# Kernel tuning notes

Measured on AMD Instinct MI355X. Metric: run time of the kernel, lower is better.

The kernel has to match this reference:

```python
import jax, jax.numpy as jnp
import numpy as np

D_MODEL = 1024
NUM_HEADS = 16
HEAD_DIM = D_MODEL // NUM_HEADS


def setup_inputs() -> dict:
    key = jax.random.key(0)
    ks = jax.random.split(key, 5)
    B, S, D_IN = 2, 2048, 1024
    x = jax.random.normal(ks[0], (B, S, D_IN), dtype=jnp.float32)
    std = 0.02
    wq = jax.random.normal(ks[1], (D_MODEL, D_IN), dtype=jnp.float32) * std
    wk = jax.random.normal(ks[2], (D_MODEL, D_IN), dtype=jnp.float32) * std
    wv = jax.random.normal(ks[3], (D_MODEL, D_IN), dtype=jnp.float32) * std
    wo = jax.random.normal(ks[4], (D_IN, D_MODEL), dtype=jnp.float32) * std
    return {"x": x, "wq": wq, "wk": wk, "wv": wv, "wo": wo}


def _mha(x, wq, wk, wv, wo):
    B, S, _ = x.shape
    H, Dh = NUM_HEADS, HEAD_DIM
    # projections: Linear applies x @ W.T with W of shape [out, in]
    q = (x @ wq.T).reshape(B, S, H, Dh).transpose(0, 2, 1, 3)  # [B,H,S,Dh]
    k = (x @ wk.T).reshape(B, S, H, Dh).transpose(0, 2, 1, 3)
    v = (x @ wv.T).reshape(B, S, H, Dh).transpose(0, 2, 1, 3)
    scores = jnp.einsum('bhqd,bhkd->bhqk', q, k) / jnp.sqrt(jnp.float32(Dh))
    causal = jnp.tril(jnp.ones((S, S), dtype=bool))  # True where attended
    scores = jnp.where(causal, scores, -jnp.inf)
    attn = jax.nn.softmax(scores, axis=-1)
    out = jnp.einsum('bhqk,bhkd->bhqd', attn, v)  # [B,H,S,Dh]
    out = out.transpose(0, 2, 1, 3).reshape(B, S, H * Dh)
    return out @ wo.T


def reference(x, wq, wk, wv, wo):
    return _mha(x, wq, wk, wv, wo)
```

## Files before the change

### kernel.cpp

```cpp
#include <hip/hip_runtime.h>
#include <hip/hip_bf16.h>
#include <stdint.h>

using bf16 = __hip_bfloat16;
typedef __attribute__((ext_vector_type(4))) short shorts4;
typedef __attribute__((ext_vector_type(8))) short short8;
typedef __attribute__((ext_vector_type(4))) float floatx4;
typedef __attribute__((ext_vector_type(4))) unsigned int uintx4;

constexpr int BATCH = 2;
constexpr int SEQ   = 2048;
constexpr int NH    = 16;
constexpr int DH    = 64;
constexpr int DM    = 1024;
constexpr int MROWS = BATCH * SEQ;
constexpr int OUTN  = MROWS * DM;
constexpr int WN    = DM * DM;

__device__ inline short bfbits(float x) {
    bf16 h = __float2bfloat16(x);
    return __builtin_bit_cast(short, h);
}

__device__ inline void async16(bf16* lds, const bf16* g) {
    __builtin_amdgcn_global_load_lds(
        (const __attribute__((address_space(1))) unsigned int*)g,
        (__attribute__((address_space(3))) unsigned int*)lds, 16, 0, 0);
}

__device__ inline void cvt8(const float* src, bf16* dst) {
    float4 f0 = *(const float4*)(src);
    float4 f1 = *(const float4*)(src + 4);
    short8 o;
    o[0] = bfbits(f0.x); o[1] = bfbits(f0.y); o[2] = bfbits(f0.z); o[3] = bfbits(f0.w);
    o[4] = bfbits(f1.x); o[5] = bfbits(f1.y); o[6] = bfbits(f1.z); o[7] = bfbits(f1.w);
    *(short8*)(dst) = o;
}

__global__ __launch_bounds__(256)
void cvt_all(const float* __restrict__ x,  const float* __restrict__ wq,
             const float* __restrict__ wk, const float* __restrict__ wv,
             const float* __restrict__ wo, bf16* __restrict__ dst,
             bf16* __restrict__ wob)
{
    const size_t i = ((size_t)blockIdx.x * 256 + threadIdx.x) * 8;
    if (i < (size_t)OUTN + 3 * WN) {
        const float* src; size_t off;
        if (i < (size_t)OUTN)               { src = x;  off = i; }
        else if (i < (size_t)OUTN + WN)     { src = wq; off = i - OUTN; }
        else if (i < (size_t)OUTN + 2 * WN) { src = wk; off = i - OUTN - WN; }
        else                                { src = wv; off = i - OUTN - 2 * (size_t)WN; }
        cvt8(src + off, dst + i);
    } else {
        const size_t off = i - OUTN - 3 * (size_t)WN;
        cvt8(wo + off, wob + off);
    }
}

__global__ __launch_bounds__(256)
void cvt_inputs(const float* __restrict__ x,  const float* __restrict__ wq,
                const float* __restrict__ wk, const float* __restrict__ wv,
                bf16* __restrict__ dst)
{
    const size_t i = ((size_t)blockIdx.x * 256 + threadIdx.x) * 8;
    const float* src; size_t off;
    if (i < (size_t)OUTN)               { src = x;  off = i; }
    else if (i < (size_t)OUTN + WN)     { src = wq; off = i - OUTN; }
    else if (i < (size_t)OUTN + 2 * WN) { src = wk; off = i - OUTN - WN; }
    else                                { src = wv; off = i - OUTN - 2 * (size_t)WN; }
    cvt8(src + off, dst + i);
}

__global__ __launch_bounds__(256)
void cvt_wo(const float* __restrict__ wo, bf16* __restrict__ dst)
{
    const size_t i = ((size_t)blockIdx.x * 256 + threadIdx.x) * 8;
    cvt8(wo + i, dst + i);
}

template<int MODE, int NT>
__global__ __launch_bounds__(256)
void gemm_mfma(const bf16* __restrict__ A,
               const bf16* __restrict__ W0, const bf16* __restrict__ W1,
               const bf16* __restrict__ W2,
               bf16* __restrict__ C0, bf16* __restrict__ C1, bf16* __restrict__ C2,
               float* __restrict__ F)
{
    constexpr int NJ = NT / 32;
    __shared__ __align__(16) bf16 As[128 * 32];
    __shared__ __align__(16) bf16 Ws[NT * 32];

    const int t    = threadIdx.x;
    const int wave = t >> 6;
    const int lane = t & 63;
    const int quad = lane >> 4;
    const int l16  = lane & 15;
    const int m0 = blockIdx.y * 128;
    const int n0 = blockIdx.x * NT;
    const int wr = (wave >> 1) * 64;
    const int wc = (wave & 1) * (NT / 2);

    const int z = (MODE == 0) ? blockIdx.z : 0;
    const bf16* W = (z == 0) ? W0 : ((z == 1) ? W1 : W2);

    const int c    = t;
    bf16* lA0 = As + c * 8;          bf16* lA1 = As + c * 8 + 2048;
    bf16* lW0 = Ws + c * 8;          bf16* lW1 = Ws + c * 8 + 2048;
    const int ar0 = m0 + (c >> 2),  ar1 = m0 + 64 + (c >> 2);
    const int nr0 = n0 + (c >> 2),  nr1 = n0 + 64 + (c >> 2);
    const int kc  = (c & 3) * 8;

    floatx4 acc[4][NJ] = {};

    for (int k0 = 0; k0 < DM; k0 += 32) {
        const bf16* gA0 = A + (size_t)ar0 * DM + k0 + kc;
        const bf16* gA1 = A + (size_t)ar1 * DM + k0 + kc;
        const bf16* gW0 = W + (size_t)nr0 * DM + k0 + kc;
        const bf16* gW1 = W + (size_t)nr1 * DM + k0 + kc;

        __syncthreads();
        async16(lA0, gA0);
        async16(lA1, gA1);
        async16(lW0, gW0);
        if (NT == 128) async16(lW1, gW1);
        __syncthreads();

        short8 af[4], wf[NJ];
        #pragma unroll
        for (int i = 0; i < 4; i++)
            af[i] = *(const short8*)(As + (wr + i * 16 + l16) * 32 + quad * 8);
        #pragma unroll
        for (int j = 0; j < NJ; j++)
            wf[j] = *(const short8*)(Ws + (wc + j * 16 + l16) * 32 + quad * 8);
        #pragma unroll
        for (int i = 0; i < 4; i++)
            #pragma unroll
            for (int j = 0; j < NJ; j++)
                acc[i][j] = __builtin_amdgcn_mfma_f32_16x16x32_bf16(af[i], wf[j], acc[i][j], 0, 0, 0);
    }

    #pragma unroll
    for (int i = 0; i < 4; i++) {
        #pragma unroll
        for (int j = 0; j < NJ; j++) {
            if (MODE == 0 && z == 2) {
                const int s0 = m0 + wr + i * 16 + quad * 4;
                const int gn = n0 + wc + j * 16 + l16;
                const int b = s0 >> 11, sr = s0 & (SEQ - 1);
                const int h = gn >> 6,  d = gn & (DH - 1);
                shorts4 pv;
                #pragma unroll
                for (int r = 0; r < 4; r++) pv[r] = bfbits(acc[i][j][r]);
                *(shorts4*)(C2 + (((size_t)(b * NH + h)) * DH + d) * SEQ + sr) = pv;
            } else {
                #pragma unroll
                for (int r = 0; r < 4; r++) {
                    const int gm = m0 + wr + i * 16 + quad * 4 + r;
                    const int gn = n0 + wc + j * 16 + l16;
                    if (MODE == 1) {
                        F[(size_t)gm * DM + gn] = acc[i][j][r];
                    } else {
                        float av = acc[i][j][r];
                        if (z == 0) av *= 0.18033688f;
                        bf16* dst = (z == 0) ? C0 : C1;
                        dst[(size_t)gm * DM + gn] = __float2bfloat16(av);
                    }
                }
            }
        }
    }
}

__global__ __launch_bounds__(256)
void attn_flash(bf16* __restrict__ Q, const bf16* __restrict__ K,
                const bf16* __restrict__ Vt)
{
    __shared__ __align__(16) bf16 Ks[128 * 64];
    __shared__ __align__(16) bf16 Vs[64 * 128];

    const int t    = threadIdx.x;
    const int wave = t >> 6;
    const int lane = t & 63;
    const int quad = lane >> 4;
    const int l16  = lane & 15;

    const int h  = blockIdx.y;
    const int b  = blockIdx.z;
    const int qt = (blockIdx.x + 5 * h + 16 * b) & 31;
    const int q0 = qt * 64;
    const int hc = h * DH;
    const size_t rowb = (size_t)b * SEQ;
    const size_t bhv  = ((size_t)(b * NH + h)) * SEQ * DH;

    const int qrow = q0 + wave * 16;
    const int qg   = qrow + l16;

    short8 qf0 = *(const short8*)(Q + (rowb + qrow + l16) * DM + hc + quad * 8);
    short8 qf1 = *(const short8*)(Q + (rowb + qrow + l16) * DM + hc + quad * 8 + 32);

    floatx4 oacc[4] = {};
    float lsum = 0.f;

    const int kx   = l16 & 7;
    const int koff0 = (quad ^ kx) * 8;
    const int koff1 = ((quad ^ 4) ^ kx) * 8;

    const int sA = (2 * (quad & 1)) * 16 + l16;
    const int sB = sA + 16;
    const bool hiTile = (quad >= 2);

    for (int k0 = 0; k0 < q0 + 64; k0 += 128) {
        __syncthreads();
        #pragma unroll
        for (int p = 0; p < 4; p++) {
            const int ck = p * 256 + t;
            const int kr = ck >> 3;
            const int kg = (ck & 7) ^ (kr & 7);
            async16(Ks + ck * 8, K + (rowb + k0 + kr) * DM + hc + kg * 8);
            const int cv = p * 256 + t;
            const int vr = cv >> 4;
            const int vg = (cv & 15) ^ (vr & 15);
            async16(Vs + cv * 8, Vt + bhv + (size_t)vr * SEQ + k0 + vg * 8);
        }
        __syncthreads();

        #pragma unroll
        for (int c64 = 0; c64 < 128; c64 += 64) {
            const int kb0 = k0 + c64;
            if (kb0 > qrow + 15) continue;

            floatx4 sc[4];
            #pragma unroll
            for (int jj = 0; jj < 4; jj++) {
                const int rowk = c64 + jj * 16 + l16;
                short8 kf0 = *(const short8*)(Ks + rowk * 64 + koff0);
                short8 kf1 = *(const short8*)(Ks + rowk * 64 + koff1);
                floatx4 cc = {};
                cc = __builtin_amdgcn_mfma_f32_16x16x32_bf16(kf0, qf0, cc, 0, 0, 0);
                cc = __builtin_amdgcn_mfma_f32_16x16x32_bf16(kf1, qf1, cc, 0, 0, 0);
                sc[jj] = cc;
            }
            if (kb0 + 63 > qrow) {
                #pragma unroll
                for (int jj = 0; jj < 4; jj++) {
                    const int kgb = kb0 + jj * 16 + quad * 4;
                    #pragma unroll
                    for (int r = 0; r < 4; r++)
                        sc[jj][r] = (kgb + r <= qg) ? sc[jj][r] : -1e30f;
                }
            }
            #pragma unroll
            for (int jj = 0; jj < 4; jj++)
                #pragma unroll
                for (int r = 0; r < 4; r++) {
                    const float p = __builtin_amdgcn_exp2f(sc[jj][r]);
                    sc[jj][r] = p;
                    lsum += p;
                }

            unsigned lo[4], hi[4];
            #pragma unroll
            for (int jj = 0; jj < 4; jj++) {
                lo[jj] = (unsigned)(unsigned short)bfbits(sc[jj][0]) |
                         ((unsigned)(unsigned short)bfbits(sc[jj][1]) << 16);
                hi[jj] = (unsigned)(unsigned short)bfbits(sc[jj][2]) |
                         ((unsigned)(unsigned short)bfbits(sc[jj][3]) << 16);
            }
            #pragma unroll
            for (int ks = 0; ks < 2; ks++) {
                unsigned d0a = __shfl((int)lo[2 * ks],     sA, 64);
                unsigned d0b = __shfl((int)lo[2 * ks + 1], sA, 64);
                unsigned d1a = __shfl((int)hi[2 * ks],     sA, 64);
                unsigned d1b = __shfl((int)hi[2 * ks + 1], sA, 64);
                unsigned d2a = __shfl((int)lo[2 * ks],     sB, 64);
                unsigned d2b = __shfl((int)lo[2 * ks + 1], sB, 64);
                unsigned d3a = __shfl((int)hi[2 * ks],     sB, 64);
                unsigned d3b = __shfl((int)hi[2 * ks + 1], sB, 64);
                uintx4 pw;
                pw[0] = hiTile ? d0b : d0a;
                pw[1] = hiTile ? d1b : d1a;
                pw[2] = hiTile ? d2b : d2a;
                pw[3] = hiTile ? d3b : d3a;
                short8 pb = __builtin_bit_cast(short8, pw);
                #pragma unroll
                for (int td = 0; td < 4; td++) {
                    const int vrow = td * 16 + l16;
                    const int vg   = ((c64 >> 3) + ks * 4 + quad) ^ l16;
                    short8 vf = *(const short8*)(Vs + vrow * 128 + vg * 8);
                    oacc[td] = __builtin_amdgcn_mfma_f32_16x16x32_bf16(vf, pb, oacc[td], 0, 0, 0);
                }
            }
        }
    }

    lsum += __shfl_xor(lsum, 16, 64);
    lsum += __shfl_xor(lsum, 32, 64);

    __syncthreads();
    bf16* T = Vs + wave * 16 * 72;
    const float invl = 1.0f / lsum;
    #pragma unroll
    for (int td = 0; td < 4; td++)
        #pragma unroll
        for (int r = 0; r < 4; r++)
            T[l16 * 72 + td * 16 + quad * 4 + r] = __float2bfloat16(oacc[td][r] * invl);
    #pragma unroll
    for (int pass = 0; pass < 2; pass++) {
        const int rq = (lane >> 3) + pass * 8;
        const int dd = (lane & 7) * 8;
        short8 v8 = *(const short8*)(T + rq * 72 + dd);
        *(short8*)(Q + (rowb + qrow + rq) * DM + hc + dd) = v8;
    }
}

extern "C" void kernel_launch(void* const* d_in, const int* in_sizes, int n_in,
                              void* d_out, int out_size, void* d_ws, size_t ws_size,
                              hipStream_t stream)
{
    const float* x  = (const float*)d_in[0];
    const float* wq = (const float*)d_in[1];
    const float* wk = (const float*)d_in[2];
    const float* wv = (const float*)d_in[3];
    const float* wo = (const float*)d_in[4];
    float* out = (float*)d_out;

    bf16* qb = (bf16*)d_ws;
    bf16* kb = qb + (size_t)OUTN;
    bf16* vb = kb + (size_t)OUTN;

    bf16* xb  = (bf16*)d_out;
    bf16* wqb = xb + (size_t)OUTN;
    bf16* wkb = wqb + WN;
    bf16* wvb = wkb + WN;

    const bool wsBig = ws_size >= (size_t)(3 * (size_t)OUTN + WN) * sizeof(bf16);

    if (wsBig) {
        bf16* wob = vb + (size_t)OUTN;
        cvt_all<<<(OUTN + 4 * WN) / (8 * 256), 256, 0, stream>>>(
            x, wq, wk, wv, wo, xb, wob);
        gemm_mfma<0, 128><<<dim3(DM / 128, MROWS / 128, 3), dim3(256), 0, stream>>>(
            xb, wqb, wkb, wvb, qb, kb, vb, nullptr);
        attn_flash<<<dim3(SEQ / 64, NH, BATCH), dim3(256), 0, stream>>>(qb, kb, vb);
        gemm_mfma<1, 64><<<dim3(DM / 64, MROWS / 128, 1), dim3(256), 0, stream>>>(
            qb, wob, nullptr, nullptr, nullptr, nullptr, nullptr, out);
    } else {
        cvt_inputs<<<(OUTN + 3 * WN) / (8 * 256), 256, 0, stream>>>(x, wq, wk, wv, xb);
        gemm_mfma<0, 128><<<dim3(DM / 128, MROWS / 128, 3), dim3(256), 0, stream>>>(
            xb, wqb, wkb, wvb, qb, kb, vb, nullptr);
        attn_flash<<<dim3(SEQ / 64, NH, BATCH), dim3(256), 0, stream>>>(qb, kb, vb);
        bf16* wob = kb;
        cvt_wo<<<WN / (8 * 256), 256, 0, stream>>>(wo, wob);
        gemm_mfma<1, 64><<<dim3(DM / 64, MROWS / 128, 1), dim3(256), 0, stream>>>(
            qb, wob, nullptr, nullptr, nullptr, nullptr, nullptr, out);
    }
}
```

Measured before the change: 185.6 us.

## Switch attention to 32x32x16 MFMA with 128-row query tiles per block

The attention kernel moves from 16x16x32 to 32x32x16 bf16 MFMA tiles. Each wave now handles 32 query rows, so a block covers 128 queries, which halves the grid and doubles K/V tile reuse per LDS load. The P-matrix relayout becomes a single xor-32 lane swap instead of eight indexed shuffles. The trade-offs are coarser causal skipping, fewer blocks (512) for occupancy and load balance, and higher accumulator register use.

```diff
diff --git a/kernel.cpp b/kernel.cpp
--- a/kernel.cpp
+++ b/kernel.cpp
@@ -6,6 +6,7 @@
 typedef __attribute__((ext_vector_type(4))) short shorts4;
 typedef __attribute__((ext_vector_type(8))) short short8;
 typedef __attribute__((ext_vector_type(4))) float floatx4;
+typedef __attribute__((ext_vector_type(16))) float floatx16;
 typedef __attribute__((ext_vector_type(4))) unsigned int uintx4;
 
 constexpr int BATCH = 2;
@@ -20,6 +21,11 @@
 __device__ inline short bfbits(float x) {
     bf16 h = __float2bfloat16(x);
     return __builtin_bit_cast(short, h);
+}
+
+__device__ inline unsigned pack2(float a, float b) {
+    return (unsigned)(unsigned short)bfbits(a) |
+           ((unsigned)(unsigned short)bfbits(b) << 16);
 }
 
 __device__ inline void async16(bf16* lds, const bf16* g) {
@@ -175,41 +181,36 @@
 void attn_flash(bf16* __restrict__ Q, const bf16* __restrict__ K,
                 const bf16* __restrict__ Vt)
 {
-    __shared__ __align__(16) bf16 Ks[128 * 64];
-    __shared__ __align__(16) bf16 Vs[64 * 128];
+    __shared__ __align__(16) bf16 smem[16384];
+    bf16* Ks = smem;
+    bf16* Vs = smem + 8192;
 
     const int t    = threadIdx.x;
     const int wave = t >> 6;
     const int lane = t & 63;
-    const int quad = lane >> 4;
-    const int l16  = lane & 15;
+    const int hi   = lane >> 5;
+    const int l32  = lane & 31;
 
     const int h  = blockIdx.y;
     const int b  = blockIdx.z;
-    const int qt = (blockIdx.x + 5 * h + 16 * b) & 31;
-    const int q0 = qt * 64;
+    const int qt = (blockIdx.x + 5 * h + 8 * b) & 15;
+    const int q0 = qt * 128;
     const int hc = h * DH;
     const size_t rowb = (size_t)b * SEQ;
     const size_t bhv  = ((size_t)(b * NH + h)) * SEQ * DH;
 
-    const int qrow = q0 + wave * 16;
-    const int qg   = qrow + l16;
-
-    short8 qf0 = *(const short8*)(Q + (rowb + qrow + l16) * DM + hc + quad * 8);
-    short8 qf1 = *(const short8*)(Q + (rowb + qrow + l16) * DM + hc + quad * 8 + 32);
-
-    floatx4 oacc[4] = {};
+    const int qrow = q0 + wave * 32;
+    const int qg   = qrow + l32;
+
+    short8 qf[4];
+    #pragma unroll
+    for (int s = 0; s < 4; s++)
+        qf[s] = *(const short8*)(Q + (rowb + qg) * DM + hc + s * 16 + hi * 8);
+
+    floatx16 oacc[2] = {};
     float lsum = 0.f;
 
-    const int kx   = l16 & 7;
-    const int koff0 = (quad ^ kx) * 8;
-    const int koff1 = ((quad ^ 4) ^ kx) * 8;
-
-    const int sA = (2 * (quad & 1)) * 16 + l16;
-    const int sB = sA + 16;
-    const bool hiTile = (quad >= 2);
-
-    for (int k0 = 0; k0 < q0 + 64; k0 += 128) {
+    for (int k0 = 0; k0 < q0 + 128; k0 += 128) {
         __syncthreads();
         #pragma unroll
         for (int p = 0; p < 4; p++) {
@@ -217,96 +218,99 @@
             const int kr = ck >> 3;
             const int kg = (ck & 7) ^ (kr & 7);
             async16(Ks + ck * 8, K + (rowb + k0 + kr) * DM + hc + kg * 8);
-            const int cv = p * 256 + t;
-            const int vr = cv >> 4;
-            const int vg = (cv & 15) ^ (vr & 15);
-            async16(Vs + cv * 8, Vt + bhv + (size_t)vr * SEQ + k0 + vg * 8);
+            const int vr = ck >> 4;
+            const int vg = (ck & 15) ^ (vr & 15);
+            async16(Vs + ck * 8, Vt + bhv + (size_t)vr * SEQ + k0 + vg * 8);
         }
         __syncthreads();
 
         #pragma unroll
         for (int c64 = 0; c64 < 128; c64 += 64) {
             const int kb0 = k0 + c64;
-            if (kb0 > qrow + 15) continue;
-
-            floatx4 sc[4];
+            if (kb0 > qrow + 31) continue;
+
             #pragma unroll
-            for (int jj = 0; jj < 4; jj++) {
-                const int rowk = c64 + jj * 16 + l16;
-                short8 kf0 = *(const short8*)(Ks + rowk * 64 + koff0);
-                short8 kf1 = *(const short8*)(Ks + rowk * 64 + koff1);
-                floatx4 cc = {};
-                cc = __builtin_amdgcn_mfma_f32_16x16x32_bf16(kf0, qf0, cc, 0, 0, 0);
-                cc = __builtin_amdgcn_mfma_f32_16x16x32_bf16(kf1, qf1, cc, 0, 0, 0);
-                sc[jj] = cc;
-            }
-            if (kb0 + 63 > qrow) {
-                #pragma unroll
-                for (int jj = 0; jj < 4; jj++) {
-                    const int kgb = kb0 + jj * 16 + quad * 4;
+            for (int kt = 0; kt < 2; kt++) {
+                const int kb = kb0 + kt * 32;
+                if (kb > qrow + 31) continue;
+
+                const int krow = c64 + kt * 32 + l32;
+                floatx16 sc = {};
+                #pragma unroll
+                for (int s = 0; s < 4; s++) {
+                    const int g = (s * 2 + hi) ^ (krow & 7);
+                    short8 kf = *(const short8*)(Ks + krow * 64 + g * 8);
+                    sc = __builtin_amdgcn_mfma_f32_32x32x16_bf16(kf, qf[s], sc, 0, 0, 0);
+                }
+
+                if (kb + 31 > qrow) {
                     #pragma unroll
-                    for (int r = 0; r < 4; r++)
-                        sc[jj][r] = (kgb + r <= qg) ? sc[jj][r] : -1e30f;
-                }
-            }
-            #pragma unroll
-            for (int jj = 0; jj < 4; jj++)
-                #pragma unroll
-                for (int r = 0; r < 4; r++) {
-                    const float p = __builtin_amdgcn_exp2f(sc[jj][r]);
-                    sc[jj][r] = p;
+                    for (int r = 0; r < 16; r++) {
+                        const int key = kb + (r & 3) + 8 * (r >> 2) + 4 * hi;
+                        sc[r] = (key <= qg) ? sc[r] : -1e30f;
+                    }
+                }
+
+                #pragma unroll
+                for (int r = 0; r < 16; r++) {
+                    const float p = __builtin_amdgcn_exp2f(sc[r]);
+                    sc[r] = p;
                     lsum += p;
                 }
 
-            unsigned lo[4], hi[4];
-            #pragma unroll
-            for (int jj = 0; jj < 4; jj++) {
-                lo[jj] = (unsigned)(unsigned short)bfbits(sc[jj][0]) |
-                         ((unsigned)(unsigned short)bfbits(sc[jj][1]) << 16);
-                hi[jj] = (unsigned)(unsigned short)bfbits(sc[jj][2]) |
-                         ((unsigned)(unsigned short)bfbits(sc[jj][3]) << 16);
-            }
-            #pragma unroll
-            for (int ks = 0; ks < 2; ks++) {
-                unsigned d0a = __shfl((int)lo[2 * ks],     sA, 64);
-                unsigned d0b = __shfl((int)lo[2 * ks + 1], sA, 64);
-                unsigned d1a = __shfl((int)hi[2 * ks],     sA, 64);
-                unsigned d1b = __shfl((int)hi[2 * ks + 1], sA, 64);
-                unsigned d2a = __shfl((int)lo[2 * ks],     sB, 64);
-                unsigned d2b = __shfl((int)lo[2 * ks + 1], sB, 64);
-                unsigned d3a = __shfl((int)hi[2 * ks],     sB, 64);
-                unsigned d3b = __shfl((int)hi[2 * ks + 1], sB, 64);
-                uintx4 pw;
-                pw[0] = hiTile ? d0b : d0a;
-                pw[1] = hiTile ? d1b : d1a;
-                pw[2] = hiTile ? d2b : d2a;
-                pw[3] = hiTile ? d3b : d3a;
-                short8 pb = __builtin_bit_cast(short8, pw);
-                #pragma unroll
-                for (int td = 0; td < 4; td++) {
-                    const int vrow = td * 16 + l16;
-                    const int vg   = ((c64 >> 3) + ks * 4 + quad) ^ l16;
-                    short8 vf = *(const short8*)(Vs + vrow * 128 + vg * 8);
-                    oacc[td] = __builtin_amdgcn_mfma_f32_16x16x32_bf16(vf, pb, oacc[td], 0, 0, 0);
+                unsigned d[4][2];
+                #pragma unroll
+                for (int g = 0; g < 4; g++) {
+                    d[g][0] = pack2(sc[4 * g + 0], sc[4 * g + 1]);
+                    d[g][1] = pack2(sc[4 * g + 2], sc[4 * g + 3]);
+                }
+
+                #pragma unroll
+                for (int h16 = 0; h16 < 2; h16++) {
+                    const unsigned a0 = d[h16 * 2][0],     a1 = d[h16 * 2][1];
+                    const unsigned b0 = d[h16 * 2 + 1][0], b1 = d[h16 * 2 + 1][1];
+                    const unsigned mine0 = hi ? b0 : a0, mine1 = hi ? b1 : a1;
+                    const unsigned give0 = hi ? a0 : b0, give1 = hi ? a1 : b1;
+                    const unsigned r0 = (unsigned)__shfl_xor((int)give0, 32, 64);
+                    const unsigned r1 = (unsigned)__shfl_xor((int)give1, 32, 64);
+                    uintx4 pw;
+                    pw[0] = hi ? r0 : mine0;
+                    pw[1] = hi ? r1 : mine1;
+                    pw[2] = hi ? mine0 : r0;
+                    pw[3] = hi ? mine1 : r1;
+                    short8 pb = __builtin_bit_cast(short8, pw);
+
+                    const int Gbase = (c64 >> 3) + kt * 4 + h16 * 2 + hi;
+                    #pragma unroll
+                    for (int tile = 0; tile < 2; tile++) {
+                        const int vrow = tile * 32 + l32;
+                        const int vg = Gbase ^ (vrow & 15);
+                        short8 vf = *(const short8*)(Vs + vrow * 128 + vg * 8);
+                        oacc[tile] = __builtin_amdgcn_mfma_f32_32x32x16_bf16(vf, pb, oacc[tile], 0, 0, 0);
+                    }
                 }
             }
         }
     }
 
-    lsum += __shfl_xor(lsum, 16, 64);
     lsum += __shfl_xor(lsum, 32, 64);
+    const float invl = 1.0f / lsum;
 
     __syncthreads();
-    bf16* T = Vs + wave * 16 * 72;
-    const float invl = 1.0f / lsum;
+    bf16* T = smem + wave * (32 * 72);
     #pragma unroll
-    for (int td = 0; td < 4; td++)
-        #pragma unroll
-        for (int r = 0; r < 4; r++)
-            T[l16 * 72 + td * 16 + quad * 4 + r] = __float2bfloat16(oacc[td][r] * invl);
+    for (int tile = 0; tile < 2; tile++)
+        #pragma unroll
+        for (int rq = 0; rq < 4; rq++) {
+            shorts4 v4;
+            #pragma unroll
+            for (int s = 0; s < 4; s++) v4[s] = bfbits(oacc[tile][rq * 4 + s] * invl);
+            *(shorts4*)(T + l32 * 72 + tile * 32 + rq * 8 + hi * 4) = v4;
+        }
+    asm volatile("s_waitcnt lgkmcnt(0)" ::: "memory");
     #pragma unroll
-    for (int pass = 0; pass < 2; pass++) {
-        const int rq = (lane >> 3) + pass * 8;
+    for (int p = 0; p < 4; p++) {
+        const int rq = (lane >> 3) + p * 8;
         const int dd = (lane & 7) * 8;
         short8 v8 = *(const short8*)(T + rq * 72 + dd);
         *(short8*)(Q + (rowb + qrow + rq) * DM + hc + dd) = v8;
@@ -341,14 +345,14 @@
             x, wq, wk, wv, wo, xb, wob);
         gemm_mfma<0, 128><<<dim3(DM / 128, MROWS / 128, 3), dim3(256), 0, stream>>>(
             xb, wqb, wkb, wvb, qb, kb, vb, nullptr);
-        attn_flash<<<dim3(SEQ / 64, NH, BATCH), dim3(256), 0, stream>>>(qb, kb, vb);
+        attn_flash<<<dim3(SEQ / 128, NH, BATCH), dim3(256), 0, stream>>>(qb, kb, vb);
         gemm_mfma<1, 64><<<dim3(DM / 64, MROWS / 128, 1), dim3(256), 0, stream>>>(
             qb, wob, nullptr, nullptr, nullptr, nullptr, nullptr, out);
     } else {
         cvt_inputs<<<(OUTN + 3 * WN) / (8 * 256), 256, 0, stream>>>(x, wq, wk, wv, xb);
         gemm_mfma<0, 128><<<dim3(DM / 128, MROWS / 128, 3), dim3(256), 0, stream>>>(
             xb, wqb, wkb, wvb, qb, kb, vb, nullptr);
-        attn_flash<<<dim3(SEQ / 64, NH, BATCH), dim3(256), 0, stream>>>(qb, kb, vb);
+        attn_flash<<<dim3(SEQ / 128, NH, BATCH), dim3(256), 0, stream>>>(qb, kb, vb);
         bf16* wob = kb;
         cvt_wo<<<WN / (8 * 256), 256, 0, stream>>>(wo, wob);
         gemm_mfma<1, 64><<<dim3(DM / 64, MROWS / 128, 1), dim3(256), 0, stream>>>(
```

Measured after the change: 191.3 us. +3.0%, slower.
